# Kernel tuning notes

Hardware: AMD Instinct MI355X
Metric: run time of the kernel (lower is better)

The kernel has to match this reference:

```python
import jax, jax.numpy as jnp
import numpy as np

HEADS, OUT = 4, 64  # GATConv(heads=4, out_channels=64, concat=False)
NEG_SLOPE = 0.2


def gat_conv(x, src, dst, num_nodes, W, att_src, att_dst, bias):
    # x: [N, Fin]; W: [Fin, H*C]; att_*: [H, C]; bias: [C]
    N = num_nodes
    H, C = att_src.shape
    h = (x @ W).reshape(N, H, C)                      # per-head projections
    a_s = jnp.einsum('nhc,hc->nh', h, att_src)        # [N, H]
    a_d = jnp.einsum('nhc,hc->nh', h, att_dst)        # [N, H]
    e = jax.nn.leaky_relu(a_s[src] + a_d[dst], NEG_SLOPE)   # [E, H]
    # segment softmax over destination nodes (self-loops guarantee nonempty segments)
    m = jax.lax.stop_gradient(jax.ops.segment_max(e, dst, num_segments=N))
    ex = jnp.exp(e - m[dst])
    den = jax.ops.segment_sum(ex, dst, num_segments=N)
    alpha = ex / den[dst]                              # [E, H]
    out = jax.ops.segment_sum(h[src] * alpha[:, :, None], dst, num_segments=N)  # [N,H,C]
    return out.mean(axis=1) + bias                     # concat=False -> head mean


def setup_inputs() -> dict:
    key = jax.random.key(0)
    ks = jax.random.split(key, 16)
    N, E, Fin, G = 100000, 800000, 8, 256
    x = jax.random.normal(ks[0], (N, Fin), dtype=jnp.float32)
    edge_index = jax.random.randint(ks[1], (2, E), 0, N, dtype=jnp.int64)
    batch = jnp.sort(jax.random.randint(ks[2], (N,), 0, G, dtype=jnp.int64))
    s = 0.1
    return {
        'x': x, 'edge_index': edge_index, 'batch': batch, 'num_graphs': G,
        'W1': jax.random.normal(ks[3], (Fin, HEADS * OUT), jnp.float32) * s,
        'a_src1': jax.random.normal(ks[4], (HEADS, OUT), jnp.float32) * s,
        'a_dst1': jax.random.normal(ks[5], (HEADS, OUT), jnp.float32) * s,
        'b1': jnp.zeros((OUT,), jnp.float32),
        'W2': jax.random.normal(ks[6], (OUT, HEADS * OUT), jnp.float32) * s,
        'a_src2': jax.random.normal(ks[7], (HEADS, OUT), jnp.float32) * s,
        'a_dst2': jax.random.normal(ks[8], (HEADS, OUT), jnp.float32) * s,
        'b2': jnp.zeros((OUT,), jnp.float32),
        'Wp1': jax.random.normal(ks[9], (OUT, 32), jnp.float32) * s,
        'bp1': jnp.zeros((32,), jnp.float32),
        'Wp2': jax.random.normal(ks[10], (32, 1), jnp.float32) * s,
        'bp2': jnp.zeros((1,), jnp.float32),
    }


def reference(x, edge_index, batch, num_graphs,
              W1, a_src1, a_dst1, b1,
              W2, a_src2, a_dst2, b2,
              Wp1, bp1, Wp2, bp2):
    N = x.shape[0]
    loops = jnp.arange(N, dtype=edge_index.dtype)
    src = jnp.concatenate([edge_index[0], loops])  # PyG add_self_loops=True
    dst = jnp.concatenate([edge_index[1], loops])
    h = jax.nn.relu(gat_conv(x, src, dst, N, W1, a_src1, a_dst1, b1))
    h = jax.nn.relu(gat_conv(h, src, dst, N, W2, a_src2, a_dst2, b2))
    # global mean pool per graph
    sums = jax.ops.segment_sum(h, batch, num_segments=num_graphs)
    cnt = jax.ops.segment_sum(jnp.ones((N,), h.dtype), batch, num_segments=num_graphs)
    pooled = sums / jnp.maximum(cnt, 1.0)[:, None]
    hid = jax.nn.relu(pooled @ Wp1 + bp1)
    return hid @ Wp2 + bp2  # [num_graphs, 1]
```

## Files before the change

### kernel.cpp

```cpp
#include <hip/hip_runtime.h>

#define HEADS 4
#define CH 64
#define HC 256
#define NEG 0.2f

typedef __attribute__((ext_vector_type(8))) short bf16x8;
typedef __attribute__((ext_vector_type(4))) float f32x4;

__device__ __forceinline__ unsigned short f2bf(float f){
  unsigned u = __float_as_uint(f);
  u += 0x7fffu + ((u >> 16) & 1u);
  return (unsigned short)(u >> 16);
}
__device__ __forceinline__ float bf2f(unsigned short s){
  return __uint_as_float(((unsigned)s) << 16);
}

__global__ __launch_bounds__(256)
void deg_count_kernel(const int* __restrict__ esrc, const int* __restrict__ edst,
                      int E, int N, int* __restrict__ deg)
{
  int e = blockIdx.x*256 + threadIdx.x;
  if (e >= E + N) return;
  int d = (e < E) ? edst[e] : e - E;
  atomicAdd(deg + d, 1);
}

__global__ __launch_bounds__(256)
void scan1_kernel(const int* __restrict__ deg, int* __restrict__ excl,
                  int* __restrict__ bsum, int N)
{
  __shared__ int sm[256];
  int i = blockIdx.x*256 + threadIdx.x;
  int v = (i < N) ? deg[i] : 0;
  sm[threadIdx.x] = v; __syncthreads();
  for (int off = 1; off < 256; off <<= 1){
    int t = (threadIdx.x >= off) ? sm[threadIdx.x - off] : 0;
    __syncthreads();
    sm[threadIdx.x] += t;
    __syncthreads();
  }
  if (i < N) excl[i] = sm[threadIdx.x] - v;
  if (threadIdx.x == 255) bsum[blockIdx.x] = sm[255];
}

__global__ __launch_bounds__(512)
void scan2_kernel(int* __restrict__ bsum, int nb)
{
  __shared__ int sm[512];
  int v = (threadIdx.x < nb) ? bsum[threadIdx.x] : 0;
  sm[threadIdx.x] = v; __syncthreads();
  for (int off = 1; off < 512; off <<= 1){
    int t = (threadIdx.x >= off) ? sm[threadIdx.x - off] : 0;
    __syncthreads();
    sm[threadIdx.x] += t;
    __syncthreads();
  }
  if (threadIdx.x < nb) bsum[threadIdx.x] = sm[threadIdx.x] - v;
}

__global__ __launch_bounds__(256)
void scan3_kernel(int* __restrict__ excl, const int* __restrict__ bsum,
                  int* __restrict__ cursor, int N)
{
  int i = blockIdx.x*256 + threadIdx.x;
  if (i >= N) return;
  int r = excl[i] + bsum[blockIdx.x];
  excl[i] = r; cursor[i] = r;
}

__global__ __launch_bounds__(256)
void scatter_kernel(const int* __restrict__ esrc, const int* __restrict__ edst,
                    int E, int N, int* __restrict__ cursor, int* __restrict__ ssrc)
{
  int e = blockIdx.x*256 + threadIdx.x;
  if (e >= E + N) return;
  int s, d;
  if (e < E){ s = esrc[e]; d = edst[e]; } else { s = d = e - E; }
  int pos = atomicAdd(cursor + d, 1);
  ssrc[pos] = s;
}

template<int FIN>
__global__ void fold_kernel(const float* __restrict__ W,
                            const float* __restrict__ att_src, const float* __restrict__ att_dst,
                            float* __restrict__ wfold)
{
  int o = threadIdx.x;
  int f = o >> 3, j = o & 7;
  int h = j & 3;
  const float* att = (j < 4) ? att_src : att_dst;
  float acc = 0.f;
#pragma unroll
  for (int c = 0; c < CH; ++c)
    acc += W[(size_t)f*HC + h*CH + c] * att[h*CH + c];
  wfold[f*8 + j] = acc;
}

template<int FIN>
__global__ __launch_bounds__(256)
void att_kernel(const float* __restrict__ x, const float* __restrict__ wfold,
                float* __restrict__ a_s, float* __restrict__ a_d, int N)
{
  __shared__ float xs[32][FIN];
  __shared__ float wf[FIN*8];
  const int t = threadIdx.x;
  const int n0 = blockIdx.x * 32;
  for (int i = t; i < FIN*8; i += 256) wf[i] = wfold[i];
  for (int i = t; i < 32*FIN; i += 256){
    int n = n0 + i / FIN;
    xs[i/FIN][i%FIN] = (n < N) ? x[(size_t)n*FIN + (i % FIN)] : 0.f;
  }
  __syncthreads();
  const int nn = t >> 3, j = t & 7;
  const int n = n0 + nn;
  if (n >= N) return;
  float acc = 0.f;
#pragma unroll
  for (int f = 0; f < FIN; ++f) acc += xs[nn][f] * wf[f*8 + j];
  if (j < 4) a_s[(size_t)n*4 + j]     = acc;
  else       a_d[(size_t)n*4 + (j-4)] = acc;
}

__global__ __launch_bounds__(256)
void att_bf_kernel(const unsigned short* __restrict__ xb, const float* __restrict__ wfold,
                   float* __restrict__ a_s, float* __restrict__ a_d, int N)
{
  __shared__ float xs[32][64];
  __shared__ float wf[64*8];
  const int t = threadIdx.x;
  const int n0 = blockIdx.x * 32;
  const ushort4* xb4 = (const ushort4*)xb;
  for (int i = t; i < 64*8; i += 256) wf[i] = wfold[i];
  for (int i4 = t; i4 < 32*16; i4 += 256){
    int n = n0 + (i4 >> 4);
    ushort4 v = (n < N) ? xb4[(size_t)n*16 + (i4 & 15)] : make_ushort4(0,0,0,0);
    float* dst = &xs[i4 >> 4][(i4 & 15)*4];
    dst[0] = bf2f(v.x); dst[1] = bf2f(v.y); dst[2] = bf2f(v.z); dst[3] = bf2f(v.w);
  }
  __syncthreads();
  const int nn = t >> 3, j = t & 7;
  const int n = n0 + nn;
  if (n >= N) return;
  float acc = 0.f;
#pragma unroll
  for (int f = 0; f < 64; ++f) acc += xs[nn][f] * wf[f*8 + j];
  if (j < 4) a_s[(size_t)n*4 + j]     = acc;
  else       a_d[(size_t)n*4 + (j-4)] = acc;
}

__global__ __launch_bounds__(256)
void gat_l1_kernel(const int* __restrict__ rowstart, const int* __restrict__ ssrc,
                   int N, int Etot,
                   const float* __restrict__ a_s, const float* __restrict__ a_d,
                   const float* __restrict__ x, const float* __restrict__ W1,
                   const float* __restrict__ b1,
                   unsigned short* __restrict__ featb)
{
  __shared__ int    slds[4][4][16];
  __shared__ float4 wlds[4][4][16];
  __shared__ float4 zlds[16][8];
  __shared__ float4 dnlds[16];
  const int t    = threadIdx.x;
  const int wv   = t >> 6;
  const int lane = t & 63;
  const int grp  = lane >> 4;
  const int fq   = lane & 15;
  const int p    = fq >> 3;
  const int f    = fq & 7;
  const int r    = wv*4 + grp;
  const int d    = blockIdx.x*16 + r;

  float z0=0.f, z1=0.f, z2=0.f, z3=0.f;
  float dn0=0.f, dn1=0.f, dn2=0.f, dn3=0.f;
  if (d < N){
    const int start = rowstart[d];
    const int end   = (d == N-1) ? Etot : rowstart[d+1];
    const float4 ad4 = *(const float4*)(a_d + (size_t)d*4);
    for (int base = start; base < end; base += 16){
      const int cnt = min(16, end - base);
      int sreg = 0; float e0=0.f, e1=0.f, e2=0.f, e3=0.f;
      if (fq < cnt){
        sreg = ssrc[base + fq];
        const float4 as4 = *(const float4*)(a_s + (size_t)sreg*4);
        float v;
        v = as4.x + ad4.x; v = v > 0.f ? v : NEG*v; e0 = __expf(v);
        v = as4.y + ad4.y; v = v > 0.f ? v : NEG*v; e1 = __expf(v);
        v = as4.z + ad4.z; v = v > 0.f ? v : NEG*v; e2 = __expf(v);
        v = as4.w + ad4.w; v = v > 0.f ? v : NEG*v; e3 = __expf(v);
      }
      slds[wv][grp][fq] = sreg;
      wlds[wv][grp][fq] = make_float4(e0, e1, e2, e3);
      __builtin_amdgcn_wave_barrier();
      for (int k = p; k < cnt; k += 2){
        const int    s  = slds[wv][grp][k];
        const float4 w4 = wlds[wv][grp][k];
        const float  xv = x[(size_t)s*8 + f];
        z0 += w4.x*xv; z1 += w4.y*xv; z2 += w4.z*xv; z3 += w4.w*xv;
        dn0 += w4.x; dn1 += w4.y; dn2 += w4.z; dn3 += w4.w;
      }
      __builtin_amdgcn_wave_barrier();
    }
  }
  z0  += __shfl_xor(z0, 8);  z1  += __shfl_xor(z1, 8);
  z2  += __shfl_xor(z2, 8);  z3  += __shfl_xor(z3, 8);
  dn0 += __shfl_xor(dn0, 8); dn1 += __shfl_xor(dn1, 8);
  dn2 += __shfl_xor(dn2, 8); dn3 += __shfl_xor(dn3, 8);
  if (d >= N){ dn0=dn1=dn2=dn3=1.f; }
  if (fq < 8)  zlds[r][f] = make_float4(z0, z1, z2, z3);
  if (fq == 0) dnlds[r]   = make_float4(dn0, dn1, dn2, dn3);
  __syncthreads();
  float Wf[4][8];
#pragma unroll
  for (int h = 0; h < 4; ++h)
#pragma unroll
    for (int ff = 0; ff < 8; ++ff)
      Wf[h][ff] = W1[ff*HC + h*CH + lane];
  const float bc = b1[lane];
#pragma unroll
  for (int i = 0; i < 4; ++i){
    const int r2 = wv*4 + i;
    const int d2 = blockIdx.x*16 + r2;
    if (d2 >= N) break;
    const float4 dn = dnlds[r2];
    float a0=0.f, a1=0.f, a2=0.f, a3=0.f;
#pragma unroll
    for (int ff = 0; ff < 8; ++ff){
      const float4 q = zlds[r2][ff];
      a0 += q.x*Wf[0][ff]; a1 += q.y*Wf[1][ff];
      a2 += q.z*Wf[2][ff]; a3 += q.w*Wf[3][ff];
    }
    float val = 0.25f*(a0*__builtin_amdgcn_rcpf(dn.x) + a1*__builtin_amdgcn_rcpf(dn.y)
                     + a2*__builtin_amdgcn_rcpf(dn.z) + a3*__builtin_amdgcn_rcpf(dn.w));
    val = fmaxf(val + bc, 0.f);
    featb[(size_t)d2*CH + lane] = f2bf(val);
  }
}

__global__ __launch_bounds__(256)
void w2fold_kernel(const float* __restrict__ W2, unsigned short* __restrict__ w2bf)
{
  int i = blockIdx.x*256 + threadIdx.x;
  int j  = i & 7;
  int l  = (i >> 3) & 63;
  int nf = (i >> 9) & 3;
  int kc = i >> 11;
  int q = kc*32 + (l >> 4)*8 + j;
  int c = nf*16 + (l & 15);
  int f = q & 63, h = q >> 6;
  w2bf[i] = f2bf(W2[(size_t)f*HC + h*64 + c]);
}

__global__ __launch_bounds__(256)
void gat_z_mfma_kernel(const int* __restrict__ rowstart, const int* __restrict__ ssrc,
                       int N, int Etot,
                       const float* __restrict__ a_s, const float* __restrict__ a_d,
                       const unsigned short* __restrict__ featb,
                       const unsigned short* __restrict__ w2bf,
                       const float* __restrict__ b2,
                       float* __restrict__ feat2)
{
  __shared__ int    slds[4][4][16];
  __shared__ float4 wlds[4][4][16];
  __shared__ unsigned short zlds[16][264];
  const int t    = threadIdx.x;
  const int wv   = t >> 6;
  const int lane = t & 63;
  const int grp  = lane >> 4;
  const int fq   = lane & 15;
  const int r    = wv*4 + grp;
  const int d    = blockIdx.x*16 + r;

  float z00=0,z01=0,z02=0,z03=0, z10=0,z11=0,z12=0,z13=0;
  float z20=0,z21=0,z22=0,z23=0, z30=0,z31=0,z32=0,z33=0;
  float dn0=1.f, dn1=1.f, dn2=1.f, dn3=1.f;
  if (d < N){
    dn0=dn1=dn2=dn3=0.f;
    const int start = rowstart[d];
    const int end   = (d == N-1) ? Etot : rowstart[d+1];
    const float4 ad4 = *(const float4*)(a_d + (size_t)d*4);
    const ushort4* __restrict__ fb4 = (const ushort4*)featb;
    for (int base = start; base < end; base += 16){
      const int cnt = min(16, end - base);
      int sreg = 0; float e0=0.f, e1=0.f, e2=0.f, e3=0.f;
      if (fq < cnt){
        sreg = ssrc[base + fq];
        const float4 as4 = *(const float4*)(a_s + (size_t)sreg*4);
        float v;
        v = as4.x + ad4.x; v = v > 0.f ? v : NEG*v; e0 = __expf(v);
        v = as4.y + ad4.y; v = v > 0.f ? v : NEG*v; e1 = __expf(v);
        v = as4.z + ad4.z; v = v > 0.f ? v : NEG*v; e2 = __expf(v);
        v = as4.w + ad4.w; v = v > 0.f ? v : NEG*v; e3 = __expf(v);
      }
      slds[wv][grp][fq] = sreg;
      wlds[wv][grp][fq] = make_float4(e0, e1, e2, e3);
      __builtin_amdgcn_wave_barrier();
      for (int k = 0; k < cnt; ++k){
        const int    s  = slds[wv][grp][k];
        const float4 w4 = wlds[wv][grp][k];
        const ushort4 hv = fb4[(size_t)s*16 + fq];
        const float f0 = bf2f(hv.x), f1 = bf2f(hv.y), f2 = bf2f(hv.z), f3 = bf2f(hv.w);
        z00 += w4.x*f0; z01 += w4.x*f1; z02 += w4.x*f2; z03 += w4.x*f3;
        z10 += w4.y*f0; z11 += w4.y*f1; z12 += w4.y*f2; z13 += w4.y*f3;
        z20 += w4.z*f0; z21 += w4.z*f1; z22 += w4.z*f2; z23 += w4.z*f3;
        z30 += w4.w*f0; z31 += w4.w*f1; z32 += w4.w*f2; z33 += w4.w*f3;
        dn0 += w4.x; dn1 += w4.y; dn2 += w4.z; dn3 += w4.w;
      }
      __builtin_amdgcn_wave_barrier();
    }
  }
  {
    const float s0 = 0.25f*__builtin_amdgcn_rcpf(dn0);
    const float s1 = 0.25f*__builtin_amdgcn_rcpf(dn1);
    const float s2 = 0.25f*__builtin_amdgcn_rcpf(dn2);
    const float s3 = 0.25f*__builtin_amdgcn_rcpf(dn3);
    ushort4* zrow = (ushort4*)zlds[r];
    ushort4 o;
    o.x=f2bf(z00*s0); o.y=f2bf(z01*s0); o.z=f2bf(z02*s0); o.w=f2bf(z03*s0);
    zrow[ 0 + fq] = o;
    o.x=f2bf(z10*s1); o.y=f2bf(z11*s1); o.z=f2bf(z12*s1); o.w=f2bf(z13*s1);
    zrow[16 + fq] = o;
    o.x=f2bf(z20*s2); o.y=f2bf(z21*s2); o.z=f2bf(z22*s2); o.w=f2bf(z23*s2);
    zrow[32 + fq] = o;
    o.x=f2bf(z30*s3); o.y=f2bf(z31*s3); o.z=f2bf(z32*s3); o.w=f2bf(z33*s3);
    zrow[48 + fq] = o;
  }
  __syncthreads();
  const bf16x8* __restrict__ bfr = (const bf16x8*)w2bf;
  const int arow = lane & 15;
  const int kg   = lane >> 4;
  f32x4 acc = {0.f, 0.f, 0.f, 0.f};
#pragma unroll
  for (int kc = 0; kc < 8; ++kc){
    const bf16x8 a = *(const bf16x8*)(&zlds[arow][kc*32 + kg*8]);
    const bf16x8 b = bfr[(kc*4 + wv)*64 + lane];
    acc = __builtin_amdgcn_mfma_f32_16x16x32_bf16(a, b, acc, 0, 0, 0);
  }
  const int col = lane & 15;
  const float bias = b2[wv*16 + col];
#pragma unroll
  for (int reg = 0; reg < 4; ++reg){
    const int rr = blockIdx.x*16 + kg*4 + reg;
    if (rr < N)
      feat2[(size_t)rr*CH + wv*16 + col] = fmaxf(acc[reg] + bias, 0.f);
  }
}

__global__ __launch_bounds__(256)
void pool_mlp_kernel(const float* __restrict__ feat,
                     const int* __restrict__ batch, int N,
                     const float* __restrict__ Wp1, const float* __restrict__ bp1,
                     const float* __restrict__ Wp2, const float* __restrict__ bp2,
                     float* __restrict__ out)
{
  const int g = blockIdx.x;
  __shared__ int seg[2];
  __shared__ float part[256];
  __shared__ float pooled[CH];
  if (threadIdx.x < 2){
    int target = g + (int)threadIdx.x;
    int lo = 0, hi = N;
    while (lo < hi){ int mid = (lo + hi) >> 1; if (batch[mid] < target) lo = mid + 1; else hi = mid; }
    seg[threadIdx.x] = lo;
  }
  __syncthreads();
  const int start = seg[0], end = seg[1];
  const int c = threadIdx.x & 63, w = threadIdx.x >> 6;
  float acc = 0.f;
  for (int n = start + w; n < end; n += 4)
    acc += feat[(size_t)n*CH + c];
  part[threadIdx.x] = acc;
  __syncthreads();
  if (threadIdx.x < CH){
    float s = part[threadIdx.x] + part[threadIdx.x+64] + part[threadIdx.x+128] + part[threadIdx.x+192];
    pooled[threadIdx.x] = s / fmaxf((float)(end - start), 1.f);
  }
  __syncthreads();
  float hid = 0.f;
  if (threadIdx.x < 32){
    float a2 = bp1[threadIdx.x];
#pragma unroll
    for (int k = 0; k < CH; ++k) a2 += pooled[k] * Wp1[k*32 + threadIdx.x];
    hid = fmaxf(a2, 0.f) * Wp2[threadIdx.x];
  }
#pragma unroll
  for (int off = 16; off; off >>= 1) hid += __shfl_down(hid, off);
  if (threadIdx.x == 0) out[g] = hid + bp2[0];
}

extern "C" void kernel_launch(void* const* d_in, const int* in_sizes, int n_in,
                              void* d_out, int out_size, void* d_ws, size_t ws_size,
                              hipStream_t stream)
{
  const float* x   = (const float*)d_in[0];
  const int*   ei  = (const int*)d_in[1];
  const int*   bat = (const int*)d_in[2];
  const float* W1  = (const float*)d_in[4];
  const float* as1 = (const float*)d_in[5];
  const float* ad1 = (const float*)d_in[6];
  const float* b1  = (const float*)d_in[7];
  const float* W2  = (const float*)d_in[8];
  const float* as2 = (const float*)d_in[9];
  const float* ad2 = (const float*)d_in[10];
  const float* b2  = (const float*)d_in[11];
  const float* Wp1 = (const float*)d_in[12];
  const float* bp1 = (const float*)d_in[13];
  const float* Wp2 = (const float*)d_in[14];
  const float* bp2 = (const float*)d_in[15];

  const int N = in_sizes[0] / 8;
  const int E = in_sizes[1] / 2;
  const int G = out_size;
  const int Etot = E + N;
  const int* esrc = ei;
  const int* edst = ei + E;

  char* wsb = (char*)d_ws;
  size_t o = 0;
  auto carve = [&](size_t bytes)->char*{
    char* p = wsb + o; o += (bytes + 255) & ~(size_t)255; return p;
  };
  unsigned short* featb = (unsigned short*)carve((size_t)N*CH*sizeof(unsigned short));
  unsigned short* w2bf  = (unsigned short*)carve((size_t)HC*CH*sizeof(unsigned short));
  float* a_s      = (float*)carve((size_t)N*HEADS*sizeof(float));
  float* a_d      = (float*)carve((size_t)N*HEADS*sizeof(float));
  float* feat2    = (float*)carve((size_t)N*CH*sizeof(float));
  float* wfold    = (float*)carve((size_t)64*8*sizeof(float));
  int*   rowstart = (int*)carve((size_t)N*sizeof(int));
  int*   cursor   = (int*)carve((size_t)N*sizeof(int));
  int*   deg      = (int*)carve((size_t)N*sizeof(int));
  int*   bsum     = (int*)carve((size_t)512*sizeof(int));
  int*   ssrc     = (int*)carve((size_t)Etot*sizeof(int));

  const int eb  = (Etot + 255) / 256;
  const int nb1 = (N + 255) / 256;
  const int atb = (N + 31) / 32;
  const int gb  = (N + 15) / 16;

  hipMemsetAsync(deg, 0, (size_t)N*sizeof(int), stream);
  deg_count_kernel<<<eb, 256, 0, stream>>>(esrc, edst, E, N, deg);
  scan1_kernel<<<nb1, 256, 0, stream>>>(deg, rowstart, bsum, N);
  scan2_kernel<<<1, 512, 0, stream>>>(bsum, nb1);
  scan3_kernel<<<nb1, 256, 0, stream>>>(rowstart, bsum, cursor, N);
  scatter_kernel<<<eb, 256, 0, stream>>>(esrc, edst, E, N, cursor, ssrc);

  fold_kernel<8><<<1, 8*8, 0, stream>>>(W1, as1, ad1, wfold);
  att_kernel<8><<<atb, 256, 0, stream>>>(x, wfold, a_s, a_d, N);
  gat_l1_kernel<<<gb, 256, 0, stream>>>(rowstart, ssrc, N, Etot, a_s, a_d, x, W1, b1, featb);

  fold_kernel<64><<<1, 64*8, 0, stream>>>(W2, as2, ad2, wfold);
  att_bf_kernel<<<atb, 256, 0, stream>>>(featb, wfold, a_s, a_d, N);
  w2fold_kernel<<<64, 256, 0, stream>>>(W2, w2bf);
  gat_z_mfma_kernel<<<gb, 256, 0, stream>>>(rowstart, ssrc, N, Etot, a_s, a_d,
                                            featb, w2bf, b2, feat2);

  pool_mlp_kernel<<<G, 256, 0, stream>>>(feat2, bat, N, Wp1, bp1, Wp2, bp2, (float*)d_out);
}
```

Baseline: 239.0 us.

## Handle self-loops analytically and range-partition CSR build atomics

Self-loop edges are no longer materialised in the CSR; each destination's self term is computed directly in both aggregation kernels from its own a_s/a_d and features. The degree-count and scatter kernels now use a grid-strided loop where each of 8 block groups handles only destinations in one slice of the node range, aiming to localise atomic traffic. The cost is that every block group rereads the full edge destination array, eight times the read traffic.

Measured after the change: 216.1 us. 1.11x faster.

```diff
diff --git a/kernel.cpp b/kernel.cpp
--- a/kernel.cpp
+++ b/kernel.cpp
@@ -18,13 +18,17 @@
 }
 
 __global__ __launch_bounds__(256)
-void deg_count_kernel(const int* __restrict__ esrc, const int* __restrict__ edst,
-                      int E, int N, int* __restrict__ deg)
-{
-  int e = blockIdx.x*256 + threadIdx.x;
-  if (e >= E + N) return;
-  int d = (e < E) ? edst[e] : e - E;
-  atomicAdd(deg + d, 1);
+void deg_count_kernel(const int* __restrict__ edst, int E, int N,
+                      int* __restrict__ deg, int cpr)
+{
+  const int range = blockIdx.x & 7;
+  const int lo = (int)(((long long)N * range) / 8);
+  const int hi = (int)(((long long)N * (range+1)) / 8);
+  const int stride = cpr * 256;
+  for (int e = (blockIdx.x >> 3)*256 + threadIdx.x; e < E; e += stride){
+    int d = edst[e];
+    if (d >= lo && d < hi) atomicAdd(deg + d, 1);
+  }
 }
 
 __global__ __launch_bounds__(256)
@@ -72,14 +76,20 @@
 
 __global__ __launch_bounds__(256)
 void scatter_kernel(const int* __restrict__ esrc, const int* __restrict__ edst,
-                    int E, int N, int* __restrict__ cursor, int* __restrict__ ssrc)
-{
-  int e = blockIdx.x*256 + threadIdx.x;
-  if (e >= E + N) return;
-  int s, d;
-  if (e < E){ s = esrc[e]; d = edst[e]; } else { s = d = e - E; }
-  int pos = atomicAdd(cursor + d, 1);
-  ssrc[pos] = s;
+                    int E, int N, int* __restrict__ cursor, int* __restrict__ ssrc,
+                    int cpr)
+{
+  const int range = blockIdx.x & 7;
+  const int lo = (int)(((long long)N * range) / 8);
+  const int hi = (int)(((long long)N * (range+1)) / 8);
+  const int stride = cpr * 256;
+  for (int e = (blockIdx.x >> 3)*256 + threadIdx.x; e < E; e += stride){
+    int d = edst[e];
+    if (d >= lo && d < hi){
+      int pos = atomicAdd(cursor + d, 1);
+      ssrc[pos] = esrc[e];
+    }
+  }
 }
 
 template<int FIN>
@@ -152,7 +162,7 @@
 
 __global__ __launch_bounds__(256)
 void gat_l1_kernel(const int* __restrict__ rowstart, const int* __restrict__ ssrc,
-                   int N, int Etot,
+                   int N, int E,
                    const float* __restrict__ a_s, const float* __restrict__ a_d,
                    const float* __restrict__ x, const float* __restrict__ W1,
                    const float* __restrict__ b1,
@@ -176,8 +186,21 @@
   float dn0=0.f, dn1=0.f, dn2=0.f, dn3=0.f;
   if (d < N){
     const int start = rowstart[d];
-    const int end   = (d == N-1) ? Etot : rowstart[d+1];
+    const int end   = (d == N-1) ? E : rowstart[d+1];
     const float4 ad4 = *(const float4*)(a_d + (size_t)d*4);
+    {
+      const float4 asd = *(const float4*)(a_s + (size_t)d*4);
+      float v, es0, es1, es2, es3;
+      v = asd.x + ad4.x; v = v > 0.f ? v : NEG*v; es0 = __expf(v);
+      v = asd.y + ad4.y; v = v > 0.f ? v : NEG*v; es1 = __expf(v);
+      v = asd.z + ad4.z; v = v > 0.f ? v : NEG*v; es2 = __expf(v);
+      v = asd.w + ad4.w; v = v > 0.f ? v : NEG*v; es3 = __expf(v);
+      if (p == 0){
+        const float xv = x[(size_t)d*8 + f];
+        z0 += es0*xv; z1 += es1*xv; z2 += es2*xv; z3 += es3*xv;
+        dn0 += es0; dn1 += es1; dn2 += es2; dn3 += es3;
+      }
+    }
     for (int base = start; base < end; base += 16){
       const int cnt = min(16, end - base);
       int sreg = 0; float e0=0.f, e1=0.f, e2=0.f, e3=0.f;
@@ -254,7 +277,7 @@
 
 __global__ __launch_bounds__(256)
 void gat_z_mfma_kernel(const int* __restrict__ rowstart, const int* __restrict__ ssrc,
-                       int N, int Etot,
+                       int N, int E,
                        const float* __restrict__ a_s, const float* __restrict__ a_d,
                        const unsigned short* __restrict__ featb,
                        const unsigned short* __restrict__ w2bf,
@@ -276,11 +299,25 @@
   float z20=0,z21=0,z22=0,z23=0, z30=0,z31=0,z32=0,z33=0;
   float dn0=1.f, dn1=1.f, dn2=1.f, dn3=1.f;
   if (d < N){
-    dn0=dn1=dn2=dn3=0.f;
     const int start = rowstart[d];
-    const int end   = (d == N-1) ? Etot : rowstart[d+1];
+    const int end   = (d == N-1) ? E : rowstart[d+1];
     const float4 ad4 = *(const float4*)(a_d + (size_t)d*4);
     const ushort4* __restrict__ fb4 = (const ushort4*)featb;
+    {
+      const float4 asd = *(const float4*)(a_s + (size_t)d*4);
+      float v, es0, es1, es2, es3;
+      v = asd.x + ad4.x; v = v > 0.f ? v : NEG*v; es0 = __expf(v);
+      v = asd.y + ad4.y; v = v > 0.f ? v : NEG*v; es1 = __expf(v);
+      v = asd.z + ad4.z; v = v > 0.f ? v : NEG*v; es2 = __expf(v);
+      v = asd.w + ad4.w; v = v > 0.f ? v : NEG*v; es3 = __expf(v);
+      const ushort4 hv = fb4[(size_t)d*16 + fq];
+      const float f0 = bf2f(hv.x), f1 = bf2f(hv.y), f2 = bf2f(hv.z), f3 = bf2f(hv.w);
+      z00 = es0*f0; z01 = es0*f1; z02 = es0*f2; z03 = es0*f3;
+      z10 = es1*f0; z11 = es1*f1; z12 = es1*f2; z13 = es1*f3;
+      z20 = es2*f0; z21 = es2*f1; z22 = es2*f2; z23 = es2*f3;
+      z30 = es3*f0; z31 = es3*f1; z32 = es3*f2; z33 = es3*f3;
+      dn0 = es0; dn1 = es1; dn2 = es2; dn3 = es3;
+    }
     for (int base = start; base < end; base += 16){
       const int cnt = min(16, end - base);
       int sreg = 0; float e0=0.f, e1=0.f, e2=0.f, e3=0.f;
@@ -412,7 +449,6 @@
   const int N = in_sizes[0] / 8;
   const int E = in_sizes[1] / 2;
   const int G = out_size;
-  const int Etot = E + N;
   const int* esrc = ei;
   const int* edst = ei + E;
 
@@ -431,28 +467,29 @@
   int*   cursor   = (int*)carve((size_t)N*sizeof(int));
   int*   deg      = (int*)carve((size_t)N*sizeof(int));
   int*   bsum     = (int*)carve((size_t)512*sizeof(int));
-  int*   ssrc     = (int*)carve((size_t)Etot*sizeof(int));
-
-  const int eb  = (Etot + 255) / 256;
+  int*   ssrc     = (int*)carve((size_t)E*sizeof(int));
+
   const int nb1 = (N + 255) / 256;
   const int atb = (N + 31) / 32;
   const int gb  = (N + 15) / 16;
+  const int cpr = 512;
+  const int csb = 8 * cpr;
 
   hipMemsetAsync(deg, 0, (size_t)N*sizeof(int), stream);
-  deg_count_kernel<<<eb, 256, 0, stream>>>(esrc, edst, E, N, deg);
+  deg_count_kernel<<<csb, 256, 0, stream>>>(edst, E, N, deg, cpr);
   scan1_kernel<<<nb1, 256, 0, stream>>>(deg, rowstart, bsum, N);
   scan2_kernel<<<1, 512, 0, stream>>>(bsum, nb1);
   scan3_kernel<<<nb1, 256, 0, stream>>>(rowstart, bsum, cursor, N);
-  scatter_kernel<<<eb, 256, 0, stream>>>(esrc, edst, E, N, cursor, ssrc);
+  scatter_kernel<<<csb, 256, 0, stream>>>(esrc, edst, E, N, cursor, ssrc, cpr);
 
   fold_kernel<8><<<1, 8*8, 0, stream>>>(W1, as1, ad1, wfold);
   att_kernel<8><<<atb, 256, 0, stream>>>(x, wfold, a_s, a_d, N);
-  gat_l1_kernel<<<gb, 256, 0, stream>>>(rowstart, ssrc, N, Etot, a_s, a_d, x, W1, b1, featb);
+  gat_l1_kernel<<<gb, 256, 0, stream>>>(rowstart, ssrc, N, E, a_s, a_d, x, W1, b1, featb);
 
   fold_kernel<64><<<1, 64*8, 0, stream>>>(W2, as2, ad2, wfold);
   att_bf_kernel<<<atb, 256, 0, stream>>>(featb, wfold, a_s, a_d, N);
   w2fold_kernel<<<64, 256, 0, stream>>>(W2, w2bf);
-  gat_z_mfma_kernel<<<gb, 256, 0, stream>>>(rowstart, ssrc, N, Etot, a_s, a_d,
+  gat_z_mfma_kernel<<<gb, 256, 0, stream>>>(rowstart, ssrc, N, E, a_s, a_d,
                                             featb, w2bf, b2, feat2);
 
   pool_mlp_kernel<<<G, 256, 0, stream>>>(feat2, bat, N, Wp1, bp1, Wp2, bp2, (float*)d_out);
```
